# Kernel tuning notes

Hardware: AMD Instinct MI355X
Metric: run time of the kernel (lower is better)

## Reference

```python
import jax, jax.numpy as jnp
import numpy as np

B, S, H, NH = 8, 2048, 768, 12
HD = H // NH  # 64

def setup_inputs() -> dict:
    key = jax.random.key(0)
    ks = jax.random.split(key, 7)
    init = 0.02
    return {
        "hidden_states": jax.random.normal(ks[0], (B, S, H), dtype=jnp.float32),
        "attention_mask": jnp.zeros((B, 1, 1, S), dtype=jnp.float32),
        "Wq": jax.random.normal(ks[1], (H, H), dtype=jnp.float32) * init,
        "bq": jnp.zeros((H,), dtype=jnp.float32),
        "Wk": jax.random.normal(ks[2], (H, H), dtype=jnp.float32) * init,
        "bk": jnp.zeros((H,), dtype=jnp.float32),
        "Wv": jax.random.normal(ks[3], (H, H), dtype=jnp.float32) * init,
        "bv": jnp.zeros((H,), dtype=jnp.float32),
    }

def reference(hidden_states, attention_mask, Wq, bq, Wk, bk, Wv, bv):
    # Linear projections (torch Linear: x @ W.T + b), then split heads -> [B,NH,S,HD]
    def heads(x):
        return x.reshape(B, S, NH, HD).transpose(0, 2, 1, 3)
    q = heads(hidden_states @ Wq.T + bq)
    k = heads(hidden_states @ Wk.T + bk)
    v = heads(hidden_states @ Wv.T + bv)
    scores = jnp.einsum('bhqd,bhkd->bhqk', q, k) / jnp.sqrt(jnp.float32(HD))
    scores = scores + attention_mask  # additive mask, broadcast [B,1,1,S]
    probs = jax.nn.softmax(scores, axis=-1)  # dropout p=0 -> identity
    ctx = jnp.einsum('bhqk,bhkd->bhqd', probs, v)
    ctx = ctx.transpose(0, 2, 1, 3).reshape(B, S, H)
    return ctx
```

## Files before the change

kernel.cpp:

```cpp
#include <hip/hip_runtime.h>

typedef __bf16 bf16_t;
typedef __bf16 bf16x8 __attribute__((ext_vector_type(8)));
typedef __bf16 bf16x4 __attribute__((ext_vector_type(4)));
typedef float  f32x4  __attribute__((ext_vector_type(4)));
typedef short  s16x4  __attribute__((ext_vector_type(4)));

#define DEV __device__ __forceinline__

#define BB 8
#define SS 2048
#define HH 768
#define NHH 12
#define HD 64
#define NX (BB*SS*HH)
#define NW (HH*HH)

DEV void gl_lds16(const void* g, void* s) {
  __builtin_amdgcn_global_load_lds(
      (__attribute__((address_space(1))) void*)(void*)g,
      (__attribute__((address_space(3))) void*)s, 16, 0, 0);
}

DEV int swz4(int r) { return (r ^ (r >> 2)) & 3; }

DEV f32x4 mfma16(bf16x4 a, bf16x4 b, f32x4 c) {
  return __builtin_amdgcn_mfma_f32_16x16x16bf16_1k(
      __builtin_bit_cast(s16x4, a), __builtin_bit_cast(s16x4, b), c, 0, 0, 0);
}

__global__ __launch_bounds__(256) void cvt_kernel(
    const float* __restrict__ X, const float* __restrict__ Wq,
    const float* __restrict__ Wk, const float* __restrict__ Wv,
    bf16_t* __restrict__ Xb, bf16_t* __restrict__ Wb) {
  int idx = (blockIdx.x * 256 + threadIdx.x) * 4;
  const float* src;
  bf16_t* dst;
  if (idx < NX) { src = X + idx; dst = Xb + idx; }
  else {
    int j = idx - NX;
    int w = j / NW;
    int jj = j - w * NW;
    src = (w == 0 ? Wq : (w == 1 ? Wk : Wv)) + jj;
    dst = Wb + j;
  }
  float4 v = *(const float4*)src;
  bf16x4 o;
  o[0] = (bf16_t)v.x; o[1] = (bf16_t)v.y; o[2] = (bf16_t)v.z; o[3] = (bf16_t)v.w;
  *(bf16x4*)dst = o;
}

__global__ __launch_bounds__(256) void qkv_gemm(
    const bf16_t* __restrict__ Xb, const bf16_t* __restrict__ Wb,
    const float* __restrict__ bq, const float* __restrict__ bk,
    const float* __restrict__ bv,
    bf16_t* __restrict__ Q, bf16_t* __restrict__ K, bf16_t* __restrict__ VT) {
  __shared__ alignas(16) bf16_t ldsA[2][128 * 32];
  __shared__ alignas(16) bf16_t ldsB[2][128 * 32];

  const int t = threadIdx.x;
  const int w = t >> 6, l = t & 63, lr = l & 15, lq = l >> 4;
  const int wr = w >> 1, wc = w & 1;
  const int m0 = blockIdx.y * 128, n0 = blockIdx.x * 128;
  const int z = blockIdx.z;
  const bf16_t* W = Wb + z * NW;
  const float* bias = (z == 0) ? bq : (z == 1) ? bk : bv;
  const float osc = (z == 0) ? 0.1803368801f : 1.0f;

  const int sl0 = t, sl1 = t + 256;
  const int ra0 = sl0 >> 2, qa0 = (sl0 & 3) ^ swz4(ra0);
  const int ra1 = sl1 >> 2, qa1 = (sl1 & 3) ^ swz4(ra1);
  const bf16_t* A0 = Xb + (m0 + ra0) * HH + qa0 * 8;
  const bf16_t* A1 = Xb + (m0 + ra1) * HH + qa1 * 8;
  const bf16_t* B0 = W + (n0 + ra0) * HH + qa0 * 8;
  const bf16_t* B1 = W + (n0 + ra1) * HH + qa1 * 8;

  f32x4 acc[4][4] = {};

  int aoff[4], boff[4];
#pragma unroll
  for (int i = 0; i < 4; ++i) {
    int Ra = wr * 64 + i * 16 + lr;
    aoff[i] = (Ra * 4 + (lq ^ swz4(Ra))) * 8;
    int Rb = wc * 64 + i * 16 + lr;
    boff[i] = (Rb * 4 + (lq ^ swz4(Rb))) * 8;
  }

  auto stage = [&](int buf, int kt) {
    int ko = kt * 32;
    gl_lds16(A0 + ko, ldsA[buf] + sl0 * 8);
    gl_lds16(A1 + ko, ldsA[buf] + sl1 * 8);
    gl_lds16(B0 + ko, ldsB[buf] + sl0 * 8);
    gl_lds16(B1 + ko, ldsB[buf] + sl1 * 8);
  };

  auto compute = [&](const int buf) {
    bf16x8 a[4], bb[4];
#pragma unroll
    for (int i = 0; i < 4; ++i) a[i] = *(const bf16x8*)(ldsA[buf] + aoff[i]);
#pragma unroll
    for (int j = 0; j < 4; ++j) bb[j] = *(const bf16x8*)(ldsB[buf] + boff[j]);
#pragma unroll
    for (int i = 0; i < 4; ++i)
#pragma unroll
      for (int j = 0; j < 4; ++j)
        acc[i][j] = __builtin_amdgcn_mfma_f32_16x16x32_bf16(a[i], bb[j], acc[i][j], 0, 0, 0);
  };

  stage(0, 0);
  __syncthreads();
  stage(1, 1);
  compute(0);
  for (int kt = 1; kt < 23; kt += 2) {
    __syncthreads();
    stage(0, kt + 1);
    compute(1);
    __syncthreads();
    stage(1, kt + 2);
    compute(0);
  }
  __syncthreads();
  compute(1);

  const int mb = m0 + wr * 64, nb = n0 + wc * 64;
#pragma unroll
  for (int j = 0; j < 4; ++j) {
    int n = nb + j * 16 + lr;
    int h = n >> 6, d = n & 63;
    float bbias = bias[n];
#pragma unroll
    for (int i = 0; i < 4; ++i) {
      int mrow = mb + i * 16 + lq * 4;
      int b = mrow >> 11, s = mrow & 2047;
      if (z == 2) {
        bf16x4 pk;
#pragma unroll
        for (int r = 0; r < 4; ++r) pk[r] = (bf16_t)(acc[i][j][r] + bbias);
        *(bf16x4*)(VT + ((size_t)(b * NHH + h) * HD + d) * SS + s) = pk;
      } else {
        bf16_t* O = (z == 0) ? Q : K;
#pragma unroll
        for (int r = 0; r < 4; ++r)
          O[((size_t)(b * NHH + h) * SS + s + r) * HD + d] = (bf16_t)((acc[i][j][r] + bbias) * osc);
      }
    }
  }
}

__global__ __launch_bounds__(256, 4) void flash_kernel(
    const bf16_t* __restrict__ Q, const bf16_t* __restrict__ K,
    const bf16_t* __restrict__ VT, const float* __restrict__ mask,
    float* __restrict__ out) {
  __shared__ alignas(16) bf16_t ldsKV[2][2][64 * 64];

  const int t = threadIdx.x;
  const int w = t >> 6, l = t & 63, lr = l & 15, lq = l >> 4;
  const int rs7 = lr & 7;
  const int bh = blockIdx.x % 96, b = bh / NHH, h = bh - b * NHH;
  const int s0 = (blockIdx.x / 96) * 128;
  const bf16_t* Qb = Q + ((size_t)bh * SS + s0) * HD;
  const bf16_t* Kb = K + (size_t)bh * SS * HD;
  const bf16_t* Vb = VT + (size_t)bh * HD * SS;
  const float* mb = mask + b * SS;

  bf16_t* qs = &ldsKV[0][0][0];
#pragma unroll
  for (int i = 0; i < 4; ++i) {
    int sl = t + i * 256;
    int r = sl >> 3, q = (sl & 7) ^ (r & 7);
    gl_lds16(Qb + r * HD + q * 8, qs + sl * 8);
  }
  __syncthreads();

  bf16x8 aq0[2], aq1[2];
#pragma unroll
  for (int qi = 0; qi < 2; ++qi) {
    int Rq = w * 32 + qi * 16 + lr;
    aq0[qi] = *(const bf16x8*)(qs + (Rq * 8 + (lq ^ (Rq & 7))) * 8);
    aq1[qi] = *(const bf16x8*)(qs + (Rq * 8 + ((lq + 4) ^ (Rq & 7))) * 8);
  }
  __syncthreads();

  const int c0 = t, c1 = t + 256;
  const int cr0 = c0 >> 3, cq0 = (c0 & 7) ^ (cr0 & 7);
  const int cr1 = c1 >> 3, cq1 = (c1 & 7) ^ (cr1 & 7);

  auto stage = [&](int buf, int kt) {
    const bf16_t* ks = Kb + kt * 64 * HD;
    gl_lds16(ks + cr0 * HD + cq0 * 8, ldsKV[buf][0] + c0 * 8);
    gl_lds16(ks + cr1 * HD + cq1 * 8, ldsKV[buf][0] + c1 * 8);
    gl_lds16(Vb + cr0 * SS + kt * 64 + cq0 * 8, ldsKV[buf][1] + c0 * 8);
    gl_lds16(Vb + cr1 * SS + kt * 64 + cq1 * 8, ldsKV[buf][1] + c1 * 8);
  };

  const char* LB = (const char*)&ldsKV[0][0][0];
  const int kb0 = lr * 128 + ((lq ^ rs7) * 16);
  const int kb1 = lr * 128 + (((lq + 4) ^ rs7) * 16);
  int vb[4];
  {
    const int vbase = lr * 128 + (((lq >> 1) ^ (rs7 & 1)) * 16) + (lq & 1) * 8;
#pragma unroll
    for (int j = 0; j < 4; ++j) vb[j] = vbase + 32 * (j ^ (rs7 >> 1));
  }

  f32x4 O[2][4] = {};
  f32x4 Lacc[2] = {};
  bf16x4 ones;
#pragma unroll
  for (int r = 0; r < 4; ++r) ones[r] = (bf16_t)1.0f;

  const float L2E = 1.44269504f;

  auto compute = [&](const int BUFB, int kt) {
    const char* Kbase = LB + BUFB;
    const char* Vbase = LB + BUFB + 8192;

    bf16x4 pb[2][4];
#pragma unroll
    for (int j = 0; j < 4; ++j) {
      bf16x8 k0 = *(const bf16x8*)(Kbase + kb0 + j * 2048);
      bf16x8 k1 = *(const bf16x8*)(Kbase + kb1 + j * 2048);
      f32x4 mvv = *(const f32x4*)(mb + kt * 64 + j * 16 + lq * 4);
      f32x4 marg = mvv * L2E;
#pragma unroll
      for (int qi = 0; qi < 2; ++qi) {
        f32x4 st = __builtin_amdgcn_mfma_f32_16x16x32_bf16(k0, aq0[qi], marg, 0, 0, 0);
        st = __builtin_amdgcn_mfma_f32_16x16x32_bf16(k1, aq1[qi], st, 0, 0, 0);
#pragma unroll
        for (int r = 0; r < 4; ++r)
          pb[qi][j][r] = (bf16_t)__builtin_amdgcn_exp2f(st[r]);
      }
    }

#pragma unroll
    for (int qi = 0; qi < 2; ++qi)
#pragma unroll
      for (int j = 0; j < 4; ++j)
        Lacc[qi] = mfma16(ones, pb[qi][j], Lacc[qi]);

#pragma unroll
    for (int dt = 0; dt < 4; ++dt) {
#pragma unroll
      for (int j = 0; j < 4; ++j) {
        bf16x4 av = *(const bf16x4*)(Vbase + vb[j] + dt * 2048);
#pragma unroll
        for (int qi = 0; qi < 2; ++qi)
          O[qi][dt] = mfma16(av, pb[qi][j], O[qi][dt]);
      }
    }
  };

  stage(0, 0);
  __syncthreads();
  stage(1, 1);
  compute(0, 0);
  for (int kt = 1; kt < 31; kt += 2) {
    __syncthreads();
    stage(0, kt + 1);
    compute(16384, kt);
    __syncthreads();
    stage(1, kt + 2);
    compute(0, kt + 1);
  }
  __syncthreads();
  compute(16384, 31);

#pragma unroll
  for (int qi = 0; qi < 2; ++qi) {
    float inv = 1.0f / Lacc[qi][0];
    int srow = s0 + w * 32 + qi * 16 + lr;
    float* op = out + ((size_t)b * SS + srow) * HH + h * HD;
#pragma unroll
    for (int dt = 0; dt < 4; ++dt) {
      f32x4 o = O[qi][dt];
      o *= inv;
      *(f32x4*)(op + dt * 16 + lq * 4) = o;
    }
  }
}

extern "C" void kernel_launch(void* const* d_in, const int* in_sizes, int n_in,
                              void* d_out, int out_size, void* d_ws, size_t ws_size,
                              hipStream_t stream) {
  const float* X    = (const float*)d_in[0];
  const float* mask = (const float*)d_in[1];
  const float* Wq   = (const float*)d_in[2];
  const float* bq   = (const float*)d_in[3];
  const float* Wk   = (const float*)d_in[4];
  const float* bk   = (const float*)d_in[5];
  const float* Wv   = (const float*)d_in[6];
  const float* bv   = (const float*)d_in[7];
  float* out = (float*)d_out;

  char* ws = (char*)d_ws;
  bf16_t* Xb = (bf16_t*)(ws);
  bf16_t* Wb = (bf16_t*)(ws + 25165824);
  bf16_t* Qb = (bf16_t*)(ws + 28704768);
  bf16_t* Kb = (bf16_t*)(ws + 53870592);
  bf16_t* VT = (bf16_t*)(ws + 79036416);

  cvt_kernel<<<14016, 256, 0, stream>>>(X, Wq, Wk, Wv, Xb, Wb);
  qkv_gemm<<<dim3(6, 128, 3), 256, 0, stream>>>(Xb, Wb, bq, bk, bv, Qb, Kb, VT);
  flash_kernel<<<1536, 256, 0, stream>>>(Qb, Kb, VT, mask, out);
}
```

Before: 352.0 us.

## Use 16x16x32 MFMA for PV via per-wave LDS repack of P

Rewrites the P·V and row-sum stages to use the 16x16x32 bf16 MFMA instead of 16x16x16. Probabilities are written to a per-wave swizzled LDS buffer and read back in the K=32 operand layout, and V is read with a matching swizzle. This halves the MFMA instruction count for PV, at the cost of extra LDS writes and reads per tile. It also relies on intra-wave ordering between the LDS writes and reads, since no barrier is added.

```diff
diff --git a/kernel.cpp b/kernel.cpp
--- a/kernel.cpp
+++ b/kernel.cpp
@@ -24,9 +24,8 @@
 
 DEV int swz4(int r) { return (r ^ (r >> 2)) & 3; }
 
-DEV f32x4 mfma16(bf16x4 a, bf16x4 b, f32x4 c) {
-  return __builtin_amdgcn_mfma_f32_16x16x16bf16_1k(
-      __builtin_bit_cast(s16x4, a), __builtin_bit_cast(s16x4, b), c, 0, 0, 0);
+DEV f32x4 mfma32(bf16x8 a, bf16x8 b, f32x4 c) {
+  return __builtin_amdgcn_mfma_f32_16x16x32_bf16(a, b, c, 0, 0, 0);
 }
 
 __global__ __launch_bounds__(256) void cvt_kernel(
@@ -152,10 +151,11 @@
     const bf16_t* __restrict__ VT, const float* __restrict__ mask,
     float* __restrict__ out) {
   __shared__ alignas(16) bf16_t ldsKV[2][2][64 * 64];
+  __shared__ alignas(16) bf16_t ldsP[4][32 * 32];
 
   const int t = threadIdx.x;
   const int w = t >> 6, l = t & 63, lr = l & 15, lq = l >> 4;
-  const int rs7 = lr & 7;
+  const int rs7 = lr & 7, rs3 = lr & 3;
   const int bh = blockIdx.x % 96, b = bh / NHH, h = bh - b * NHH;
   const int s0 = (blockIdx.x / 96) * 128;
   const bf16_t* Qb = Q + ((size_t)bh * SS + s0) * HD;
@@ -196,18 +196,19 @@
   const char* LB = (const char*)&ldsKV[0][0][0];
   const int kb0 = lr * 128 + ((lq ^ rs7) * 16);
   const int kb1 = lr * 128 + (((lq + 4) ^ rs7) * 16);
-  int vb[4];
-  {
-    const int vbase = lr * 128 + (((lq >> 1) ^ (rs7 & 1)) * 16) + (lq & 1) * 8;
-#pragma unroll
-    for (int j = 0; j < 4; ++j) vb[j] = vbase + 32 * (j ^ (rs7 >> 1));
-  }
+  int vg[2];
+#pragma unroll
+  for (int g = 0; g < 2; ++g) vg[g] = lr * 128 + (((g * 4 + lq) ^ rs7) * 16);
+  char* PWb = (char*)&ldsP[0][0] + w * 2048 + lr * 64 + (lq & 1) * 8;
+  char* PW0 = PWb + ((((lq >> 1)) ^ rs3) * 16);
+  char* PW1 = PWb + (((2 + (lq >> 1)) ^ rs3) * 16);
+  const char* PR = (const char*)&ldsP[0][0] + w * 2048 + lr * 64 + ((lq ^ rs3) * 16);
 
   f32x4 O[2][4] = {};
   f32x4 Lacc[2] = {};
-  bf16x4 ones;
-#pragma unroll
-  for (int r = 0; r < 4; ++r) ones[r] = (bf16_t)1.0f;
+  bf16x8 ones8;
+#pragma unroll
+  for (int r = 0; r < 8; ++r) ones8[r] = (bf16_t)1.0f;
 
   const float L2E = 1.44269504f;
 
@@ -215,37 +216,35 @@
     const char* Kbase = LB + BUFB;
     const char* Vbase = LB + BUFB + 8192;
 
-    bf16x4 pb[2][4];
-#pragma unroll
-    for (int j = 0; j < 4; ++j) {
-      bf16x8 k0 = *(const bf16x8*)(Kbase + kb0 + j * 2048);
-      bf16x8 k1 = *(const bf16x8*)(Kbase + kb1 + j * 2048);
-      f32x4 mvv = *(const f32x4*)(mb + kt * 64 + j * 16 + lq * 4);
-      f32x4 marg = mvv * L2E;
-#pragma unroll
-      for (int qi = 0; qi < 2; ++qi) {
-        f32x4 st = __builtin_amdgcn_mfma_f32_16x16x32_bf16(k0, aq0[qi], marg, 0, 0, 0);
-        st = __builtin_amdgcn_mfma_f32_16x16x32_bf16(k1, aq1[qi], st, 0, 0, 0);
-#pragma unroll
-        for (int r = 0; r < 4; ++r)
-          pb[qi][j][r] = (bf16_t)__builtin_amdgcn_exp2f(st[r]);
+#pragma unroll
+    for (int g = 0; g < 2; ++g) {
+#pragma unroll
+      for (int jj = 0; jj < 2; ++jj) {
+        const int j = g * 2 + jj;
+        bf16x8 k0 = *(const bf16x8*)(Kbase + kb0 + j * 2048);
+        bf16x8 k1 = *(const bf16x8*)(Kbase + kb1 + j * 2048);
+        f32x4 mvv = *(const f32x4*)(mb + kt * 64 + j * 16 + lq * 4);
+        f32x4 marg = mvv * L2E;
+#pragma unroll
+        for (int qi = 0; qi < 2; ++qi) {
+          f32x4 st = mfma32(k0, aq0[qi], marg);
+          st = mfma32(k1, aq1[qi], st);
+          bf16x4 p4;
+#pragma unroll
+          for (int r = 0; r < 4; ++r)
+            p4[r] = (bf16_t)__builtin_amdgcn_exp2f(st[r]);
+          *(bf16x4*)((jj == 0 ? PW0 : PW1) + qi * 1024) = p4;
+        }
       }
-    }
-
-#pragma unroll
-    for (int qi = 0; qi < 2; ++qi)
-#pragma unroll
-      for (int j = 0; j < 4; ++j)
-        Lacc[qi] = mfma16(ones, pb[qi][j], Lacc[qi]);
-
-#pragma unroll
-    for (int dt = 0; dt < 4; ++dt) {
-#pragma unroll
-      for (int j = 0; j < 4; ++j) {
-        bf16x4 av = *(const bf16x4*)(Vbase + vb[j] + dt * 2048);
-#pragma unroll
-        for (int qi = 0; qi < 2; ++qi)
-          O[qi][dt] = mfma16(av, pb[qi][j], O[qi][dt]);
+      bf16x8 p0 = *(const bf16x8*)(PR);
+      bf16x8 p1 = *(const bf16x8*)(PR + 1024);
+      Lacc[0] = mfma32(ones8, p0, Lacc[0]);
+      Lacc[1] = mfma32(ones8, p1, Lacc[1]);
+#pragma unroll
+      for (int dt = 0; dt < 4; ++dt) {
+        bf16x8 av = *(const bf16x8*)(Vbase + vg[g] + dt * 2048);
+        O[0][dt] = mfma32(av, p0, O[0][dt]);
+        O[1][dt] = mfma32(av, p1, O[1][dt]);
       }
     }
   };
```

After: 361.9 us. +2.8%, slower.
